# Kernel tuning notes

Measured on AMD Instinct MI355X. Metric: run time of the kernel, lower is better.

The kernel has to match this reference:

```python
import jax, jax.numpy as jnp
import numpy as np

NEG_INF = -1e30
NEG_SLOPE = 0.2


def setup_inputs() -> dict:
    key = jax.random.key(0)
    k1, k2, k3, k4, k5 = jax.random.split(key, 5)
    B, N, D, H = 2, 2048, 512, 8
    k = D // H
    return {
        "x": jax.random.normal(k1, (B, N, D), dtype=jnp.float32),
        "A": jax.random.randint(k2, (B, N, N), 0, 2, dtype=jnp.int32),
        "W_proj": jax.random.normal(k3, (D, D), dtype=jnp.float32) * (1.0 / np.sqrt(D)),
        "W_att": jax.random.normal(k4, (H, 2 * k), dtype=jnp.float32) * (1.0 / np.sqrt(2 * k)),
        "b_att": jax.random.normal(k5, (H,), dtype=jnp.float32) * 0.01,
    }


def reference(x, A, W_proj, W_att, b_att):
    # x: [B, N, D_in]; A: [B, N, N]; W_proj: [D_in, D_out]; W_att: [H, 2k]; b_att: [H]
    B, N, _ = x.shape
    H, two_k = W_att.shape
    k = two_k // 2
    xp = jnp.einsum('bnd,do->bno', x, W_proj)            # [B, N, H*k]
    xh = xp.reshape(B, N, H, k).transpose(0, 2, 1, 3)    # [B, H, N, k]
    # Additive attention: score(i,j) = leaky_relu(w[:k]@x_i + w[k:]@x_j + b).
    # Decompose instead of materializing the O(N^2 * 2k) concat tensor.
    a_src = jnp.einsum('bhnk,hk->bhn', xh, W_att[:, :k])  # contribution of node i
    a_dst = jnp.einsum('bhnk,hk->bhn', xh, W_att[:, k:])  # contribution of node j
    scores = a_src[:, :, :, None] + a_dst[:, :, None, :] + b_att[None, :, None, None]
    scores = jax.nn.leaky_relu(scores, negative_slope=NEG_SLOPE)  # [B, H, N, N]
    mask = (A > 0)[:, None, :, :]
    scores = jnp.where(mask, scores, NEG_INF)
    att = jax.nn.softmax(scores, axis=-1)
    out = jax.nn.relu(jnp.einsum('bhij,bhjk->bhik', att, xh))  # [B, H, N, k]
    return out.transpose(0, 2, 1, 3).reshape(B, N, H * k)
```

## Files before the change

kernel.cpp:

```cpp
#include <hip/hip_runtime.h>
#include <cstdint>
#include <cstddef>

#define NEG_SLOPE 0.2f
#define LOG2E 1.4426950408889634f

#define BB 2
#define NN 2048
#define DD 512
#define HH 8
#define KK 64

typedef _Float16 half8 __attribute__((ext_vector_type(8)));
typedef _Float16 half4 __attribute__((ext_vector_type(4)));
typedef _Float16 half2v __attribute__((ext_vector_type(2)));
typedef float floatx4 __attribute__((ext_vector_type(4)));

#define X16T_OFF  ((size_t)0)
#define WT_OFF    ((size_t)4194304)
#define XHT_OFF   ((size_t)4718592)
#define ASRC_OFF  ((size_t)8912896)
#define AF_OFF    ((size_t)9043968)
#define ADMAX_OFF ((size_t)9175040)
#define MW_OFF    ((size_t)9183232)

#if __has_builtin(__builtin_amdgcn_global_load_lds)
#define GLL(gsrc, lbase, lane) \
    __builtin_amdgcn_global_load_lds((const __attribute__((address_space(1))) void*)(gsrc), \
                                     (__attribute__((address_space(3))) void*)(lbase), 16, 0, 0)
#else
#define GLL(gsrc, lbase, lane) \
    (*(uint4*)((char*)(lbase) + (size_t)(lane) * 16) = *(const uint4*)(gsrc))
#endif

__global__ __launch_bounds__(256) void k_pm(const int* __restrict__ A,
                                            const float* __restrict__ x,
                                            const float* __restrict__ Wp,
                                            unsigned long long* __restrict__ mwT,
                                            _Float16* __restrict__ x16t,
                                            _Float16* __restrict__ WT) {
    __shared__ float tile[64][65];
    __shared__ unsigned long long mwt[32][4];
    const int tid = threadIdx.x;
    const int bi = blockIdx.x;
    if (bi < 1024) {
        const int w = tid >> 6, lane = tid & 63;
        const int b = bi >> 9, n0 = (bi & 511) * 4;
        const int* Arow = A + ((size_t)b * NN + n0 + w) * NN + lane;
        int v[32];
#pragma unroll
        for (int c = 0; c < 32; ++c) v[c] = Arow[c * 64];
#pragma unroll
        for (int c = 0; c < 32; ++c) {
            unsigned long long m = __ballot(v[c] != 0);
            if (lane == 0) mwt[c][w] = m;
        }
        __syncthreads();
        if (tid < 128) {
            const int c = tid >> 2, rl = tid & 3;
            mwT[((size_t)b * 32 + c) * NN + n0 + rl] = mwt[c][rl];
        }
    } else if (bi < 1280) {
        const int xb = bi - 1024;
        const int r = tid & 15, cg = tid >> 4;
        const float* srow = x + (size_t)(xb * 16 + r) * DD;
        _Float16* obase = x16t + ((size_t)xb * 64) * 128 + r * 8;
#pragma unroll
        for (int q = 0; q < 4; ++q) {
            const int chunk = q * 16 + cg;
            float4 v0 = *(const float4*)(srow + chunk * 8);
            float4 v1 = *(const float4*)(srow + chunk * 8 + 4);
            half8 hv;
            hv[0] = (_Float16)v0.x; hv[1] = (_Float16)v0.y;
            hv[2] = (_Float16)v0.z; hv[3] = (_Float16)v0.w;
            hv[4] = (_Float16)v1.x; hv[5] = (_Float16)v1.y;
            hv[6] = (_Float16)v1.z; hv[7] = (_Float16)v1.w;
            *(half8*)(obase + (size_t)chunk * 128) = hv;
        }
    } else {
        const int wb = bi - 1280;
        const int d0 = (wb >> 3) * 64, o0 = (wb & 7) * 64;
        const int r = tid >> 2, cq = tid & 3;
#pragma unroll
        for (int qq = 0; qq < 4; ++qq) {
            float4 v = *(const float4*)&Wp[(size_t)(d0 + r) * DD + o0 + cq * 16 + qq * 4];
            tile[r][cq * 16 + qq * 4 + 0] = v.x;
            tile[r][cq * 16 + qq * 4 + 1] = v.y;
            tile[r][cq * 16 + qq * 4 + 2] = v.z;
            tile[r][cq * 16 + qq * 4 + 3] = v.w;
        }
        __syncthreads();
#pragma unroll
        for (int qq = 0; qq < 2; ++qq) {
            half8 hv;
#pragma unroll
            for (int e = 0; e < 8; ++e) hv[e] = (_Float16)tile[cq * 16 + qq * 8 + e][r];
            *(half8*)&WT[(size_t)(o0 + r) * DD + d0 + cq * 16 + qq * 8] = hv;
        }
    }
}

__global__ __launch_bounds__(256) void k_proj(const _Float16* __restrict__ x16t,
                                              const _Float16* __restrict__ WT,
                                              const float* __restrict__ Watt,
                                              _Float16* __restrict__ xhT2,
                                              float* __restrict__ asrc,
                                              unsigned* __restrict__ aFg,
                                              float* __restrict__ admax) {
    __shared__ __align__(16) _Float16 bt[64 * 512];
    const int tid = threadIdx.x;
    const int bi = blockIdx.x;
    const int mtile = bi >> 3, h = bi & 7;
    const int m0 = mtile * 64;
    {
        const int cir = tid & 63, wv4 = tid >> 6;
        const char* gsrc = (const char*)(WT + (size_t)h * 64 * DD);
        char* lbase = (char*)bt;
#pragma unroll
        for (int q = 0; q < 16; ++q) {
            const int row = q * 4 + wv4;
            *(uint4*)(lbase + row * 1024 + ((cir ^ (row & 7)) * 16)) =
                *(const uint4*)(gsrc + (size_t)row * 1024 + cir * 16);
        }
    }
    __syncthreads();
    const int w = tid >> 6, l = tid & 63, li = l & 15, p = l >> 4;
    const char* bbase = (const char*)bt;
    const _Float16* abase = x16t + ((size_t)(mtile * 4 + w)) * 64 * 128 + li * 8;
    floatx4 acc[4] = {};
    for (int k0 = 0; k0 < DD; k0 += 32) {
        const int ch = (k0 >> 3) + p;
        half8 a = *(const half8*)(abase + (size_t)ch * 128);
#pragma unroll
        for (int ct = 0; ct < 4; ++ct) {
            const int row = ct * 16 + li;
            half8 bfr = *(const half8*)(bbase + row * 1024 + ((ch ^ (li & 7)) * 16));
            acc[ct] = __builtin_amdgcn_mfma_f32_16x16x32_f16(a, bfr, acc[ct], 0, 0, 0);
        }
    }
    const int b = m0 >> 11, n0m = m0 & (NN - 1);
    const int c = n0m >> 6;
    const int bh = b * HH + h;
    {
        char* tb2 = (char*)xhT2 + ((size_t)(bh * 32 + c)) * 8192;
        const int colchunk = w * 2 + (p >> 1);
        const int sub = (p & 1) * 8;
#pragma unroll
        for (int ct = 0; ct < 4; ++ct) {
            const int kk = ct * 16 + li;
            half4 hv;
#pragma unroll
            for (int r = 0; r < 4; ++r) hv[r] = (_Float16)acc[ct][r];
            *(half4*)(tb2 + kk * 128 + ((colchunk ^ (kk & 7)) << 4) + sub) = hv;
        }
    }
    float w1[4], w2[4];
#pragma unroll
    for (int ct = 0; ct < 4; ++ct) {
        w1[ct] = Watt[h * 128 + ct * 16 + li];
        w2[ct] = Watt[h * 128 + 64 + ct * 16 + li];
    }
    float mx = -1e30f;
#pragma unroll
    for (int r = 0; r < 4; ++r) {
        float s1 = 0.f, s2 = 0.f;
#pragma unroll
        for (int ct = 0; ct < 4; ++ct) { s1 += acc[ct][r] * w1[ct]; s2 += acc[ct][r] * w2[ct]; }
#pragma unroll
        for (int d = 1; d < 16; d <<= 1) { s1 += __shfl_xor(s1, d, 64); s2 += __shfl_xor(s2, d, 64); }
        mx = fmaxf(mx, s2);
        if (li == 0) {
            const int n = n0m + w * 16 + p * 4 + r;
            asrc[bh * NN + n] = s1;
            const float bj = s2 * LOG2E;
            union { half2v h; unsigned u; } cv;
            cv.h[0] = (_Float16)exp2f(bj);
            cv.h[1] = (_Float16)exp2f(NEG_SLOPE * bj);
            aFg[bh * NN + n] = cv.u;
        }
    }
    mx = fmaxf(mx, __shfl_xor(mx, 16, 64));
    mx = fmaxf(mx, __shfl_xor(mx, 32, 64));
    if (l == 0) admax[bh * 128 + (mtile & 31) * 4 + w] = mx;
}

__global__ __launch_bounds__(256) void k_attn(const _Float16* __restrict__ xhT2,
                                              const float* __restrict__ asrc,
                                              const unsigned* __restrict__ aFg,
                                              const float* __restrict__ admax,
                                              const unsigned long long* __restrict__ mwT,
                                              const float* __restrict__ batt,
                                              float* __restrict__ out) {
    __shared__ __align__(16) _Float16 vt[2][2][4096];
    __shared__ __align__(16) unsigned aFl[2][2][64];
    __shared__ unsigned long long mwl[2][2][32];
    __shared__ float accd_s[2][16];
    __shared__ float amx_s;

    const int tid = threadIdx.x;
    const int w = tid >> 6, l = tid & 63, li = l & 15, p = l >> 4;
    const int g = w & 1, wr = w >> 1;
    const int bid = blockIdx.x;
    const int bh = bid >> 6, it = bid & 63;
    const int b = bh >> 3, h = bh & (HH - 1);
    const int i0 = it * 32;

    const _Float16* vbase = xhT2 + (size_t)bh * 32 * 4096;

    {
        const int c0 = g;
#pragma unroll
        for (int q = 0; q < 4; ++q) {
            const int chunk = (wr * 4 + q) * 64 + l;
            GLL(vbase + (size_t)c0 * 4096 + chunk * 8, &vt[g][0][(wr * 4 + q) * 512], l);
        }
        if (tid < 128) aFl[tid >> 6][0][tid & 63] =
            aFg[bh * NN + (tid >> 6) * 64 + (tid & 63)];
        if (tid < 64) mwl[tid >> 5][0][tid & 31] =
            mwT[((size_t)b * 32 + (tid >> 5)) * NN + i0 + (tid & 31)];
    }
    if (w == 0) {
        float mx = fmaxf(admax[bh * 128 + l], admax[bh * 128 + 64 + l]);
#pragma unroll
        for (int d = 1; d < 64; d <<= 1) mx = fmaxf(mx, __shfl_xor(mx, d, 64));
        if (l == 0) amx_s = mx;
    }
    __syncthreads();

    const float am = amx_s;
    const float bbv = batt[h];
    const int i = i0 + wr * 16 + li;
    const float ai = (asrc[bh * NN + i] + bbv) * LOG2E;
    const float tb = ai + am * LOG2E;
    const float Mi = fmaxf(tb, NEG_SLOPE * tb);
    half2v eh2;
    eh2[0] = (_Float16)exp2f(ai - Mi);
    eh2[1] = (_Float16)exp2f(NEG_SLOPE * ai - Mi);
    floatx4 acc[4] = {};
    floatx4 accd = {};
    half8 ones;
#pragma unroll
    for (int e = 0; e < 8; ++e) ones[e] = (_Float16)1.0f;

    unsigned raF = 0; unsigned long long rmw = 0;
    for (int ci = 0; ci < 16; ++ci) {
        const int buf = ci & 1;
        char* vtg = (char*)&vt[g][buf][0];
        if (ci < 15) {
            const int cn = 2 * (ci + 1) + g;
#pragma unroll
            for (int q = 0; q < 4; ++q) {
                const int chunk = (wr * 4 + q) * 64 + l;
                GLL(vbase + (size_t)cn * 4096 + chunk * 8, &vt[g][buf ^ 1][(wr * 4 + q) * 512], l);
            }
            if (tid < 128) raF = aFg[bh * NN + (2 * (ci + 1) + (tid >> 6)) * 64 + (tid & 63)];
            if (tid < 64)  rmw = mwT[((size_t)b * 32 + 2 * (ci + 1) + (tid >> 5)) * NN + i0 + (tid & 31)];
        }
        const unsigned long long mword = mwl[g][buf][wr * 16 + li];
#pragma unroll
        for (int js = 0; js < 2; ++js) {
            const int shbase = js * 32 + p * 8;
            uint4 F0 = *(const uint4*)&aFl[g][buf][shbase];
            uint4 F1 = *(const uint4*)&aFl[g][buf][shbase + 4];
            const unsigned m8 = (unsigned)(mword >> shbase) & 0xFFu;
            unsigned fb[8] = {F0.x, F0.y, F0.z, F0.w, F1.x, F1.y, F1.z, F1.w};
            half8 af;
#pragma unroll
            for (int e = 0; e < 8; ++e) {
                union { unsigned u; half2v h; } cv; cv.u = fb[e];
                half2v em = eh2 * cv.h;
                _Float16 wv = em[0] > em[1] ? em[0] : em[1];
                af[e] = ((m8 >> e) & 1u) ? wv : (_Float16)0.f;
            }
            accd = __builtin_amdgcn_mfma_f32_16x16x32_f16(af, ones, accd, 0, 0, 0);
#pragma unroll
            for (int ct = 0; ct < 4; ++ct) {
                const half8 bf = *(const half8*)(vtg + (ct * 16 + li) * 128 +
                                                 (((js * 4 + p) ^ (li & 7)) << 4));
                acc[ct] = __builtin_amdgcn_mfma_f32_16x16x32_f16(af, bf, acc[ct], 0, 0, 0);
            }
        }
        if (ci < 15) {
            if (tid < 128) aFl[tid >> 6][buf ^ 1][tid & 63] = raF;
            if (tid < 64)  mwl[tid >> 5][buf ^ 1][tid & 31] = rmw;
        }
        __syncthreads();
    }

    float* accs = (float*)&vt[0][0][0];
    if (g == 1) {
#pragma unroll
        for (int ct = 0; ct < 4; ++ct)
#pragma unroll
            for (int r = 0; r < 4; ++r)
                accs[(wr * 16 + p * 4 + r) * 64 + ct * 16 + li] = acc[ct][r];
        if (li == 0) {
#pragma unroll
            for (int r = 0; r < 4; ++r) accd_s[wr][p * 4 + r] = accd[r];
        }
    }
    __syncthreads();
    if (g == 0) {
#pragma unroll
        for (int r = 0; r < 4; ++r) {
            const float d = accd[r] + accd_s[wr][p * 4 + r];
            const float inv = 1.f / fmaxf(d, 1e-30f);
            const int irow = i0 + wr * 16 + p * 4 + r;
            float* orow = out + ((size_t)b * NN + irow) * DD + h * KK;
#pragma unroll
            for (int ct = 0; ct < 4; ++ct) {
                const float v = (acc[ct][r] + accs[(wr * 16 + p * 4 + r) * 64 + ct * 16 + li]) * inv;
                orow[ct * 16 + li] = fmaxf(v, 0.f);
            }
        }
    }
}

extern "C" void kernel_launch(void* const* d_in, const int* in_sizes, int n_in,
                              void* d_out, int out_size, void* d_ws, size_t ws_size,
                              hipStream_t stream) {
    const float* x    = (const float*)d_in[0];
    const int*   A    = (const int*)d_in[1];
    const float* Wp   = (const float*)d_in[2];
    const float* Watt = (const float*)d_in[3];
    const float* batt = (const float*)d_in[4];
    float* out = (float*)d_out;

    char* ws = (char*)d_ws;
    _Float16* x16t = (_Float16*)(ws + X16T_OFF);
    _Float16* WT   = (_Float16*)(ws + WT_OFF);
    _Float16* xhT2 = (_Float16*)(ws + XHT_OFF);
    float* asrc  = (float*)(ws + ASRC_OFF);
    unsigned* aFg = (unsigned*)(ws + AF_OFF);
    float* admax = (float*)(ws + ADMAX_OFF);
    unsigned long long* mwT = (unsigned long long*)(ws + MW_OFF);

    k_pm<<<dim3(1344), 256, 0, stream>>>(A, x, Wp, mwT, x16t, WT);
    k_proj<<<dim3(512), 256, 0, stream>>>(x16t, WT, Watt, xhT2, asrc, aFg, admax);
    k_attn<<<dim3(BB * HH * 64), 256, 0, stream>>>(xhT2, asrc, aFg, admax, mwT, batt, out);
}
```

Measured before the change: 50.35 us.

## Process 64 query rows per attention block to reuse staged V tiles

The attention kernel now gives each block 64 query rows instead of 32, so each wave computes two 16-row fragments against the same shared-memory V tile and the same neighbor-factor data. This halves the grid and halves the number of times each V chunk is loaded into LDS and read from it per query row. The trade-off is twice the accumulator registers per wave and only 512 blocks, which may lower occupancy and latency hiding.

```diff
diff --git a/kernel.cpp b/kernel.cpp
--- a/kernel.cpp
+++ b/kernel.cpp
@@ -193,31 +193,30 @@
                                               float* __restrict__ out) {
     __shared__ __align__(16) _Float16 vt[2][2][4096];
     __shared__ __align__(16) unsigned aFl[2][2][64];
-    __shared__ unsigned long long mwl[2][2][32];
-    __shared__ float accd_s[2][16];
+    __shared__ unsigned long long mwl[2][2][64];
+    __shared__ float accd_s[2][32];
     __shared__ float amx_s;
 
     const int tid = threadIdx.x;
     const int w = tid >> 6, l = tid & 63, li = l & 15, p = l >> 4;
     const int g = w & 1, wr = w >> 1;
     const int bid = blockIdx.x;
-    const int bh = bid >> 6, it = bid & 63;
+    const int bh = bid >> 5, it = bid & 31;
     const int b = bh >> 3, h = bh & (HH - 1);
-    const int i0 = it * 32;
+    const int i0 = it * 64;
 
     const _Float16* vbase = xhT2 + (size_t)bh * 32 * 4096;
 
     {
-        const int c0 = g;
 #pragma unroll
         for (int q = 0; q < 4; ++q) {
             const int chunk = (wr * 4 + q) * 64 + l;
-            GLL(vbase + (size_t)c0 * 4096 + chunk * 8, &vt[g][0][(wr * 4 + q) * 512], l);
+            GLL(vbase + (size_t)g * 4096 + chunk * 8, &vt[g][0][(wr * 4 + q) * 512], l);
         }
         if (tid < 128) aFl[tid >> 6][0][tid & 63] =
             aFg[bh * NN + (tid >> 6) * 64 + (tid & 63)];
-        if (tid < 64) mwl[tid >> 5][0][tid & 31] =
-            mwT[((size_t)b * 32 + (tid >> 5)) * NN + i0 + (tid & 31)];
+        if (tid < 128) mwl[tid >> 6][0][tid & 63] =
+            mwT[((size_t)b * 32 + (tid >> 6)) * NN + i0 + (tid & 63)];
     }
     if (w == 0) {
         float mx = fmaxf(admax[bh * 128 + l], admax[bh * 128 + 64 + l]);
@@ -227,17 +226,19 @@
     }
     __syncthreads();
 
-    const float am = amx_s;
+    const float amL = amx_s * LOG2E;
     const float bbv = batt[h];
-    const int i = i0 + wr * 16 + li;
-    const float ai = (asrc[bh * NN + i] + bbv) * LOG2E;
-    const float tb = ai + am * LOG2E;
-    const float Mi = fmaxf(tb, NEG_SLOPE * tb);
-    half2v eh2;
-    eh2[0] = (_Float16)exp2f(ai - Mi);
-    eh2[1] = (_Float16)exp2f(NEG_SLOPE * ai - Mi);
-    floatx4 acc[4] = {};
-    floatx4 accd = {};
+    const int ia = i0 + wr * 32 + li;
+    const float aia = (asrc[bh * NN + ia] + bbv) * LOG2E;
+    const float aib = (asrc[bh * NN + ia + 16] + bbv) * LOG2E;
+    const float tba = aia + amL, tbb = aib + amL;
+    const float Mia = fmaxf(tba, NEG_SLOPE * tba);
+    const float Mib = fmaxf(tbb, NEG_SLOPE * tbb);
+    half2v eh2a, eh2b;
+    eh2a[0] = (_Float16)exp2f(aia - Mia); eh2a[1] = (_Float16)exp2f(NEG_SLOPE * aia - Mia);
+    eh2b[0] = (_Float16)exp2f(aib - Mib); eh2b[1] = (_Float16)exp2f(NEG_SLOPE * aib - Mib);
+    floatx4 acc0[4] = {}, acc1[4] = {};
+    floatx4 accd0 = {}, accd1 = {};
     half8 ones;
 #pragma unroll
     for (int e = 0; e < 8; ++e) ones[e] = (_Float16)1.0f;
@@ -254,35 +255,42 @@
                 GLL(vbase + (size_t)cn * 4096 + chunk * 8, &vt[g][buf ^ 1][(wr * 4 + q) * 512], l);
             }
             if (tid < 128) raF = aFg[bh * NN + (2 * (ci + 1) + (tid >> 6)) * 64 + (tid & 63)];
-            if (tid < 64)  rmw = mwT[((size_t)b * 32 + 2 * (ci + 1) + (tid >> 5)) * NN + i0 + (tid & 31)];
-        }
-        const unsigned long long mword = mwl[g][buf][wr * 16 + li];
+            if (tid < 128) rmw = mwT[((size_t)b * 32 + 2 * (ci + 1) + (tid >> 6)) * NN + i0 + (tid & 63)];
+        }
+        const unsigned long long mw0 = mwl[g][buf][wr * 32 + li];
+        const unsigned long long mw1 = mwl[g][buf][wr * 32 + 16 + li];
 #pragma unroll
         for (int js = 0; js < 2; ++js) {
             const int shbase = js * 32 + p * 8;
             uint4 F0 = *(const uint4*)&aFl[g][buf][shbase];
             uint4 F1 = *(const uint4*)&aFl[g][buf][shbase + 4];
-            const unsigned m8 = (unsigned)(mword >> shbase) & 0xFFu;
+            const unsigned m80 = (unsigned)(mw0 >> shbase) & 0xFFu;
+            const unsigned m81 = (unsigned)(mw1 >> shbase) & 0xFFu;
             unsigned fb[8] = {F0.x, F0.y, F0.z, F0.w, F1.x, F1.y, F1.z, F1.w};
-            half8 af;
+            half8 af0, af1;
 #pragma unroll
             for (int e = 0; e < 8; ++e) {
                 union { unsigned u; half2v h; } cv; cv.u = fb[e];
-                half2v em = eh2 * cv.h;
-                _Float16 wv = em[0] > em[1] ? em[0] : em[1];
-                af[e] = ((m8 >> e) & 1u) ? wv : (_Float16)0.f;
-            }
-            accd = __builtin_amdgcn_mfma_f32_16x16x32_f16(af, ones, accd, 0, 0, 0);
+                half2v em0 = eh2a * cv.h;
+                half2v em1 = eh2b * cv.h;
+                _Float16 w0 = em0[0] > em0[1] ? em0[0] : em0[1];
+                _Float16 w1v = em1[0] > em1[1] ? em1[0] : em1[1];
+                af0[e] = ((m80 >> e) & 1u) ? w0 : (_Float16)0.f;
+                af1[e] = ((m81 >> e) & 1u) ? w1v : (_Float16)0.f;
+            }
+            accd0 = __builtin_amdgcn_mfma_f32_16x16x32_f16(af0, ones, accd0, 0, 0, 0);
+            accd1 = __builtin_amdgcn_mfma_f32_16x16x32_f16(af1, ones, accd1, 0, 0, 0);
 #pragma unroll
             for (int ct = 0; ct < 4; ++ct) {
                 const half8 bf = *(const half8*)(vtg + (ct * 16 + li) * 128 +
                                                  (((js * 4 + p) ^ (li & 7)) << 4));
-                acc[ct] = __builtin_amdgcn_mfma_f32_16x16x32_f16(af, bf, acc[ct], 0, 0, 0);
+                acc0[ct] = __builtin_amdgcn_mfma_f32_16x16x32_f16(af0, bf, acc0[ct], 0, 0, 0);
+                acc1[ct] = __builtin_amdgcn_mfma_f32_16x16x32_f16(af1, bf, acc1[ct], 0, 0, 0);
             }
         }
         if (ci < 15) {
             if (tid < 128) aFl[tid >> 6][buf ^ 1][tid & 63] = raF;
-            if (tid < 64)  mwl[tid >> 5][buf ^ 1][tid & 31] = rmw;
+            if (tid < 128) mwl[tid >> 6][buf ^ 1][tid & 63] = rmw;
         }
         __syncthreads();
     }
@@ -292,25 +300,35 @@
 #pragma unroll
         for (int ct = 0; ct < 4; ++ct)
 #pragma unroll
-            for (int r = 0; r < 4; ++r)
-                accs[(wr * 16 + p * 4 + r) * 64 + ct * 16 + li] = acc[ct][r];
+            for (int r = 0; r < 4; ++r) {
+                accs[(wr * 32 + p * 4 + r) * 64 + ct * 16 + li] = acc0[ct][r];
+                accs[(wr * 32 + 16 + p * 4 + r) * 64 + ct * 16 + li] = acc1[ct][r];
+            }
         if (li == 0) {
 #pragma unroll
-            for (int r = 0; r < 4; ++r) accd_s[wr][p * 4 + r] = accd[r];
+            for (int r = 0; r < 4; ++r) {
+                accd_s[wr][p * 4 + r] = accd0[r];
+                accd_s[wr][16 + p * 4 + r] = accd1[r];
+            }
         }
     }
     __syncthreads();
     if (g == 0) {
 #pragma unroll
-        for (int r = 0; r < 4; ++r) {
-            const float d = accd[r] + accd_s[wr][p * 4 + r];
-            const float inv = 1.f / fmaxf(d, 1e-30f);
-            const int irow = i0 + wr * 16 + p * 4 + r;
-            float* orow = out + ((size_t)b * NN + irow) * DD + h * KK;
-#pragma unroll
-            for (int ct = 0; ct < 4; ++ct) {
-                const float v = (acc[ct][r] + accs[(wr * 16 + p * 4 + r) * 64 + ct * 16 + li]) * inv;
-                orow[ct * 16 + li] = fmaxf(v, 0.f);
+        for (int f = 0; f < 2; ++f) {
+#pragma unroll
+            for (int r = 0; r < 4; ++r) {
+                const floatx4* accf = f ? acc1 : acc0;
+                const float da = (f ? accd1[r] : accd0[r]) + accd_s[wr][f * 16 + p * 4 + r];
+                const float inv = 1.f / fmaxf(da, 1e-30f);
+                const int irow = i0 + wr * 32 + f * 16 + p * 4 + r;
+                float* orow = out + ((size_t)b * NN + irow) * DD + h * KK;
+#pragma unroll
+                for (int ct = 0; ct < 4; ++ct) {
+                    const float v = (accf[ct][r] +
+                                     accs[(wr * 32 + f * 16 + p * 4 + r) * 64 + ct * 16 + li]) * inv;
+                    orow[ct * 16 + li] = fmaxf(v, 0.f);
+                }
             }
         }
     }
@@ -337,5 +355,5 @@
 
     k_pm<<<dim3(1344), 256, 0, stream>>>(A, x, Wp, mwT, x16t, WT);
     k_proj<<<dim3(512), 256, 0, stream>>>(x16t, WT, Watt, xhT2, asrc, aFg, admax);
-    k_attn<<<dim3(BB * HH * 64), 256, 0, stream>>>(xhT2, asrc, aFg, admax, mwT, batt, out);
+    k_attn<<<dim3(BB * HH * 32), 256, 0, stream>>>(xhT2, asrc, aFg, admax, mwT, batt, out);
 }
```

After: 54.02 us. +7.3%, slower.

## Move adjacency bitmask packing into projection kernel and pack attention weights as half2

Applied to the files above, without the earlier changes.

The adjacency-to-bitmask conversion moves out of the first prep kernel and into the projection kernel, interleaved 2:1 with projection blocks. The bandwidth-bound A read can then overlap with the MFMA projection work, and the prep kernel shrinks. The per-node exp factors are split into separate positive and negative-slope arrays laid out pairwise, so the attention inner loop builds weights with packed half2 multiply/max and a bitmask AND instead of per-element selects. Risks are more block imbalance in the merged kernel, since ballot blocks are light, and 64KB of static shared memory limiting occupancy.

```diff
diff --git a/kernel.cpp b/kernel.cpp
--- a/kernel.cpp
+++ b/kernel.cpp
@@ -20,7 +20,8 @@
 #define WT_OFF    ((size_t)4194304)
 #define XHT_OFF   ((size_t)4718592)
 #define ASRC_OFF  ((size_t)8912896)
-#define AF_OFF    ((size_t)9043968)
+#define AFP_OFF   ((size_t)9043968)
+#define AFM_OFF   ((size_t)9109504)
 #define ADMAX_OFF ((size_t)9175040)
 #define MW_OFF    ((size_t)9183232)
 
@@ -33,38 +34,26 @@
     (*(uint4*)((char*)(lbase) + (size_t)(lane) * 16) = *(const uint4*)(gsrc))
 #endif
 
-__global__ __launch_bounds__(256) void k_pm(const int* __restrict__ A,
-                                            const float* __restrict__ x,
-                                            const float* __restrict__ Wp,
-                                            unsigned long long* __restrict__ mwT,
-                                            _Float16* __restrict__ x16t,
-                                            _Float16* __restrict__ WT) {
+__device__ __forceinline__ unsigned pkmm(unsigned Ep2, unsigned fp,
+                                         unsigned Em2, unsigned fm) {
+    union U { unsigned u; half2v h; };
+    U a, b, c, d, r;
+    a.u = Ep2; b.u = fp; c.u = Em2; d.u = fm;
+    r.h = __builtin_elementwise_max(a.h * b.h, c.h * d.h);
+    return r.u;
+}
+
+__global__ __launch_bounds__(256) void k_prep(const float* __restrict__ x,
+                                              const float* __restrict__ Wp,
+                                              _Float16* __restrict__ x16t,
+                                              _Float16* __restrict__ WT) {
     __shared__ float tile[64][65];
-    __shared__ unsigned long long mwt[32][4];
     const int tid = threadIdx.x;
     const int bi = blockIdx.x;
-    if (bi < 1024) {
-        const int w = tid >> 6, lane = tid & 63;
-        const int b = bi >> 9, n0 = (bi & 511) * 4;
-        const int* Arow = A + ((size_t)b * NN + n0 + w) * NN + lane;
-        int v[32];
-#pragma unroll
-        for (int c = 0; c < 32; ++c) v[c] = Arow[c * 64];
-#pragma unroll
-        for (int c = 0; c < 32; ++c) {
-            unsigned long long m = __ballot(v[c] != 0);
-            if (lane == 0) mwt[c][w] = m;
-        }
-        __syncthreads();
-        if (tid < 128) {
-            const int c = tid >> 2, rl = tid & 3;
-            mwT[((size_t)b * 32 + c) * NN + n0 + rl] = mwt[c][rl];
-        }
-    } else if (bi < 1280) {
-        const int xb = bi - 1024;
+    if (bi < 256) {
         const int r = tid & 15, cg = tid >> 4;
-        const float* srow = x + (size_t)(xb * 16 + r) * DD;
-        _Float16* obase = x16t + ((size_t)xb * 64) * 128 + r * 8;
+        const float* srow = x + (size_t)(bi * 16 + r) * DD;
+        _Float16* obase = x16t + ((size_t)bi * 64) * 128 + r * 8;
 #pragma unroll
         for (int q = 0; q < 4; ++q) {
             const int chunk = q * 16 + cg;
@@ -78,7 +67,7 @@
             *(half8*)(obase + (size_t)chunk * 128) = hv;
         }
     } else {
-        const int wb = bi - 1280;
+        const int wb = bi - 256;
         const int d0 = (wb >> 3) * 64, o0 = (wb & 7) * 64;
         const int r = tid >> 2, cq = tid & 3;
 #pragma unroll
@@ -100,17 +89,46 @@
     }
 }
 
-__global__ __launch_bounds__(256) void k_proj(const _Float16* __restrict__ x16t,
-                                              const _Float16* __restrict__ WT,
-                                              const float* __restrict__ Watt,
-                                              _Float16* __restrict__ xhT2,
-                                              float* __restrict__ asrc,
-                                              unsigned* __restrict__ aFg,
-                                              float* __restrict__ admax) {
-    __shared__ __align__(16) _Float16 bt[64 * 512];
+__global__ __launch_bounds__(256) void k_pj(const int* __restrict__ A,
+                                            const _Float16* __restrict__ x16t,
+                                            const _Float16* __restrict__ WT,
+                                            const float* __restrict__ Watt,
+                                            unsigned long long* __restrict__ mwT,
+                                            _Float16* __restrict__ xhT2,
+                                            float* __restrict__ asrc,
+                                            unsigned* __restrict__ aFp_g,
+                                            unsigned* __restrict__ aFm_g,
+                                            float* __restrict__ admax) {
+    __shared__ __align__(16) char smem[65536];
     const int tid = threadIdx.x;
     const int bi = blockIdx.x;
-    const int mtile = bi >> 3, h = bi & 7;
+    const int r3 = bi % 3;
+
+    if (r3 != 2) {
+        unsigned long long (*mwt)[4] = (unsigned long long (*)[4])smem;
+        const int mid = (bi / 3) * 2 + r3;
+        const int w = tid >> 6, lane = tid & 63;
+        const int b = mid >> 9, n0 = (mid & 511) * 4;
+        const int* Arow = A + ((size_t)b * NN + n0 + w) * NN + lane;
+        int v[32];
+#pragma unroll
+        for (int c = 0; c < 32; ++c) v[c] = Arow[c * 64];
+#pragma unroll
+        for (int c = 0; c < 32; ++c) {
+            unsigned long long m = __ballot(v[c] != 0);
+            if (lane == 0) mwt[c][w] = m;
+        }
+        __syncthreads();
+        if (tid < 128) {
+            const int c = tid >> 2, rl = tid & 3;
+            mwT[((size_t)b * 32 + c) * NN + n0 + rl] = mwt[c][rl];
+        }
+        return;
+    }
+
+    _Float16* bt = (_Float16*)smem;
+    const int pid = bi / 3;
+    const int mtile = pid >> 3, h = pid & 7;
     const int m0 = mtile * 64;
     {
         const int cir = tid & 63, wv4 = tid >> 6;
@@ -160,6 +178,7 @@
         w1[ct] = Watt[h * 128 + ct * 16 + li];
         w2[ct] = Watt[h * 128 + 64 + ct * 16 + li];
     }
+    float s1v[4], s2v[4];
     float mx = -1e30f;
 #pragma unroll
     for (int r = 0; r < 4; ++r) {
@@ -168,31 +187,43 @@
         for (int ct = 0; ct < 4; ++ct) { s1 += acc[ct][r] * w1[ct]; s2 += acc[ct][r] * w2[ct]; }
 #pragma unroll
         for (int d = 1; d < 16; d <<= 1) { s1 += __shfl_xor(s1, d, 64); s2 += __shfl_xor(s2, d, 64); }
+        s1v[r] = s1; s2v[r] = s2;
         mx = fmaxf(mx, s2);
-        if (li == 0) {
-            const int n = n0m + w * 16 + p * 4 + r;
-            asrc[bh * NN + n] = s1;
-            const float bj = s2 * LOG2E;
-            union { half2v h; unsigned u; } cv;
-            cv.h[0] = (_Float16)exp2f(bj);
-            cv.h[1] = (_Float16)exp2f(NEG_SLOPE * bj);
-            aFg[bh * NN + n] = cv.u;
-        }
     }
     mx = fmaxf(mx, __shfl_xor(mx, 16, 64));
     mx = fmaxf(mx, __shfl_xor(mx, 32, 64));
     if (l == 0) admax[bh * 128 + (mtile & 31) * 4 + w] = mx;
+    if (li == 0) {
+        const int nb = n0m + w * 16 + p * 4;
+        *(float4*)&asrc[bh * NN + nb] = make_float4(s1v[0], s1v[1], s1v[2], s1v[3]);
+        union { half2v h; unsigned u; } q;
+        unsigned fpw[2], fmw[2];
+#pragma unroll
+        for (int pr = 0; pr < 2; ++pr) {
+            q.h[0] = (_Float16)exp2f(s2v[2 * pr] * LOG2E);
+            q.h[1] = (_Float16)exp2f(s2v[2 * pr + 1] * LOG2E);
+            fpw[pr] = q.u;
+            q.h[0] = (_Float16)exp2f(NEG_SLOPE * s2v[2 * pr] * LOG2E);
+            q.h[1] = (_Float16)exp2f(NEG_SLOPE * s2v[2 * pr + 1] * LOG2E);
+            fmw[pr] = q.u;
+        }
+        const int wb = (bh * NN + nb) >> 1;
+        *(uint2*)&aFp_g[wb] = make_uint2(fpw[0], fpw[1]);
+        *(uint2*)&aFm_g[wb] = make_uint2(fmw[0], fmw[1]);
+    }
 }
 
 __global__ __launch_bounds__(256) void k_attn(const _Float16* __restrict__ xhT2,
                                               const float* __restrict__ asrc,
-                                              const unsigned* __restrict__ aFg,
+                                              const unsigned* __restrict__ aFp,
+                                              const unsigned* __restrict__ aFm,
                                               const float* __restrict__ admax,
                                               const unsigned long long* __restrict__ mwT,
                                               const float* __restrict__ batt,
                                               float* __restrict__ out) {
     __shared__ __align__(16) _Float16 vt[2][2][4096];
-    __shared__ __align__(16) unsigned aFl[2][2][64];
+    __shared__ __align__(16) unsigned aFpl[2][2][32];
+    __shared__ __align__(16) unsigned aFml[2][2][32];
     __shared__ unsigned long long mwl[2][2][32];
     __shared__ float accd_s[2][16];
     __shared__ float amx_s;
@@ -208,14 +239,16 @@
     const _Float16* vbase = xhT2 + (size_t)bh * 32 * 4096;
 
     {
-        const int c0 = g;
 #pragma unroll
         for (int q = 0; q < 4; ++q) {
             const int chunk = (wr * 4 + q) * 64 + l;
-            GLL(vbase + (size_t)c0 * 4096 + chunk * 8, &vt[g][0][(wr * 4 + q) * 512], l);
-        }
-        if (tid < 128) aFl[tid >> 6][0][tid & 63] =
-            aFg[bh * NN + (tid >> 6) * 64 + (tid & 63)];
+            GLL(vbase + (size_t)g * 4096 + chunk * 8, &vt[g][0][(wr * 4 + q) * 512], l);
+        }
+        if (tid < 128) {
+            const int arr = tid >> 6, par = (tid >> 5) & 1, wd = tid & 31;
+            const unsigned v = (arr ? aFm : aFp)[bh * 1024 + par * 32 + wd];
+            if (arr) aFml[par][0][wd] = v; else aFpl[par][0][wd] = v;
+        }
         if (tid < 64) mwl[tid >> 5][0][tid & 31] =
             mwT[((size_t)b * 32 + (tid >> 5)) * NN + i0 + (tid & 31)];
     }
@@ -233,45 +266,52 @@
     const float ai = (asrc[bh * NN + i] + bbv) * LOG2E;
     const float tb = ai + am * LOG2E;
     const float Mi = fmaxf(tb, NEG_SLOPE * tb);
-    half2v eh2;
-    eh2[0] = (_Float16)exp2f(ai - Mi);
-    eh2[1] = (_Float16)exp2f(NEG_SLOPE * ai - Mi);
+    union { half2v h; unsigned u; } epk, emk;
+    epk.h[0] = epk.h[1] = (_Float16)exp2f(ai - Mi);
+    emk.h[0] = emk.h[1] = (_Float16)exp2f(NEG_SLOPE * ai - Mi);
+    const unsigned Ep2 = epk.u, Em2 = emk.u;
     floatx4 acc[4] = {};
     floatx4 accd = {};
     half8 ones;
 #pragma unroll
     for (int e = 0; e < 8; ++e) ones[e] = (_Float16)1.0f;
 
-    unsigned raF = 0; unsigned long long rmw = 0;
+    unsigned raf = 0; unsigned long long rmw = 0;
     for (int ci = 0; ci < 16; ++ci) {
         const int buf = ci & 1;
         char* vtg = (char*)&vt[g][buf][0];
         if (ci < 15) {
-            const int cn = 2 * (ci + 1) + g;
+            const int cb = 2 * (ci + 1);
+            const int cn = cb + g;
 #pragma unroll
             for (int q = 0; q < 4; ++q) {
                 const int chunk = (wr * 4 + q) * 64 + l;
                 GLL(vbase + (size_t)cn * 4096 + chunk * 8, &vt[g][buf ^ 1][(wr * 4 + q) * 512], l);
             }
-            if (tid < 128) raF = aFg[bh * NN + (2 * (ci + 1) + (tid >> 6)) * 64 + (tid & 63)];
-            if (tid < 64)  rmw = mwT[((size_t)b * 32 + 2 * (ci + 1) + (tid >> 5)) * NN + i0 + (tid & 31)];
+            if (tid < 128) {
+                const int arr = tid >> 6, par = (tid >> 5) & 1, wd = tid & 31;
+                raf = (arr ? aFm : aFp)[bh * 1024 + (cb + par) * 32 + wd];
+            }
+            if (tid < 64) rmw = mwT[((size_t)b * 32 + cb + (tid >> 5)) * NN + i0 + (tid & 31)];
         }
         const unsigned long long mword = mwl[g][buf][wr * 16 + li];
 #pragma unroll
         for (int js = 0; js < 2; ++js) {
-            const int shbase = js * 32 + p * 8;
-            uint4 F0 = *(const uint4*)&aFl[g][buf][shbase];
-            uint4 F1 = *(const uint4*)&aFl[g][buf][shbase + 4];
-            const unsigned m8 = (unsigned)(mword >> shbase) & 0xFFu;
-            unsigned fb[8] = {F0.x, F0.y, F0.z, F0.w, F1.x, F1.y, F1.z, F1.w};
-            half8 af;
-#pragma unroll
-            for (int e = 0; e < 8; ++e) {
-                union { unsigned u; half2v h; } cv; cv.u = fb[e];
-                half2v em = eh2 * cv.h;
-                _Float16 wv = em[0] > em[1] ? em[0] : em[1];
-                af[e] = ((m8 >> e) & 1u) ? wv : (_Float16)0.f;
-            }
+            const int wb = js * 16 + p * 4;
+            const uint4 Fp4 = *(const uint4*)&aFpl[g][buf][wb];
+            const uint4 Fm4 = *(const uint4*)&aFml[g][buf][wb];
+            const unsigned m8 = (unsigned)(mword >> (js * 32 + p * 8)) & 0xFFu;
+            const unsigned fpv[4] = {Fp4.x, Fp4.y, Fp4.z, Fp4.w};
+            const unsigned fmv[4] = {Fm4.x, Fm4.y, Fm4.z, Fm4.w};
+            union { unsigned u[4]; half8 h; } afu;
+#pragma unroll
+            for (int pi = 0; pi < 4; ++pi) {
+                const unsigned m2 = (m8 >> (2 * pi)) & 3u;
+                const unsigned mk = ((m2 & 1u) ? 0x0000FFFFu : 0u) |
+                                    ((m2 & 2u) ? 0xFFFF0000u : 0u);
+                afu.u[pi] = pkmm(Ep2, fpv[pi], Em2, fmv[pi]) & mk;
+            }
+            const half8 af = afu.h;
             accd = __builtin_amdgcn_mfma_f32_16x16x32_f16(af, ones, accd, 0, 0, 0);
 #pragma unroll
             for (int ct = 0; ct < 4; ++ct) {
@@ -281,8 +321,11 @@
             }
         }
         if (ci < 15) {
-            if (tid < 128) aFl[tid >> 6][buf ^ 1][tid & 63] = raF;
-            if (tid < 64)  mwl[tid >> 5][buf ^ 1][tid & 31] = rmw;
+            if (tid < 128) {
+                const int arr = tid >> 6, par = (tid >> 5) & 1, wd = tid & 31;
+                if (arr) aFml[par][buf ^ 1][wd] = raf; else aFpl[par][buf ^ 1][wd] = raf;
+            }
+            if (tid < 64) mwl[tid >> 5][buf ^ 1][tid & 31] = rmw;
         }
         __syncthreads();
     }
@@ -331,11 +374,12 @@
     _Float16* WT   = (_Float16*)(ws + WT_OFF);
     _Float16* xhT2 = (_Float16*)(ws + XHT_OFF);
     float* asrc  = (float*)(ws + ASRC_OFF);
-    unsigned* aFg = (unsigned*)(ws + AF_OFF);
+    unsigned* aFp = (unsigned*)(ws + AFP_OFF);
+    unsigned* aFm = (unsigned*)(ws + AFM_OFF);
     float* admax = (float*)(ws + ADMAX_OFF);
     unsigned long long* mwT = (unsigned long long*)(ws + MW_OFF);
 
-    k_pm<<<dim3(1344), 256, 0, stream>>>(A, x, Wp, mwT, x16t, WT);
-    k_proj<<<dim3(512), 256, 0, stream>>>(x16t, WT, Watt, xhT2, asrc, aFg, admax);
-    k_attn<<<dim3(BB * HH * 64), 256, 0, stream>>>(xhT2, asrc, aFg, admax, mwT, batt, out);
-}
+    k_prep<<<dim3(320), 256, 0, stream>>>(x, Wp, x16t, WT);
+    k_pj<<<dim3(1536), 256, 0, stream>>>(A, x16t, WT, Watt, mwT, xhT2, asrc, aFp, aFm, admax);
+    k_attn<<<dim3(BB * HH * 64), 256, 0, stream>>>(xhT2, asrc, aFp, aFm, admax, mwT, batt, out);
+}
```

Result: slower. 51.67 us (+2.6%).
